# Performance work log

Measured on AMD Instinct MI355X. Metric: run time of the kernel, lower is better.

## Reference

```python
import jax, jax.numpy as jnp
import numpy as np
import math

NUM_BUCKETS = 32
MAX_DISTANCE = 128
N_HEADS = 16
D_KV = 64


def _relative_position_bucket(relative_position, num_buckets=NUM_BUCKETS, max_distance=MAX_DISTANCE):
    # bidirectional (encoder) variant
    num_buckets //= 2
    relative_buckets = (relative_position > 0).astype(jnp.int32) * num_buckets
    rp = jnp.abs(relative_position)
    max_exact = num_buckets // 2
    is_small = rp < max_exact
    rp_large = max_exact + (
        jnp.log(jnp.maximum(rp, 1).astype(jnp.float32) / max_exact)
        / math.log(max_distance / max_exact)
        * (num_buckets - max_exact)
    ).astype(jnp.int32)
    rp_large = jnp.minimum(rp_large, num_buckets - 1)
    return relative_buckets + jnp.where(is_small, rp, rp_large)


def compute_bias(rel_bias, q_len, k_len):
    ctx = jnp.arange(q_len)[:, None]
    mem = jnp.arange(k_len)[None, :]
    buckets = _relative_position_bucket(mem - ctx)          # [q, k]
    values = rel_bias[buckets]                               # [q, k, h]
    return jnp.transpose(values, (2, 0, 1))[None]            # [1, h, q, k]


def setup_inputs() -> dict:
    key = jax.random.key(0)
    ks = jax.random.split(key, 6)
    d_model, inner = 1024, N_HEADS * D_KV
    s = 0.02
    return {
        "hidden_states": jax.random.normal(ks[0], (2, 2048, d_model), jnp.float32),
        "Wq": jax.random.normal(ks[1], (d_model, inner), jnp.float32) * s,
        "Wk": jax.random.normal(ks[2], (d_model, inner), jnp.float32) * s,
        "Wv": jax.random.normal(ks[3], (d_model, inner), jnp.float32) * s,
        "Wo": jax.random.normal(ks[4], (inner, d_model), jnp.float32) * s,
        "rel_bias": jax.random.normal(ks[5], (NUM_BUCKETS, N_HEADS), jnp.float32) * s,
    }


def reference(hidden_states, Wq, Wk, Wv, Wo, rel_bias):
    B, S, D = hidden_states.shape

    def split_heads(x):  # [B,S,inner] -> [B,H,S,dk]
        return x.reshape(B, S, N_HEADS, D_KV).transpose(0, 2, 1, 3)

    q = split_heads(hidden_states @ Wq)
    k = split_heads(hidden_states @ Wk)
    v = split_heads(hidden_states @ Wv)

    # T5 does NOT scale by 1/sqrt(d_kv)
    scores = jnp.einsum("bhqd,bhkd->bhqk", q, k)
    scores = scores + compute_bias(rel_bias, S, S)
    attn = jax.nn.softmax(scores, axis=-1)
    ctx = jnp.einsum("bhqk,bhkd->bhqd", attn, v)
    ctx = ctx.transpose(0, 2, 1, 3).reshape(B, S, N_HEADS * D_KV)
    return ctx @ Wo
```

## Files before the change

### kernel.cpp

```cpp
#include <hip/hip_runtime.h>
#include <hip/hip_bf16.h>

typedef __bf16 bf16x8 __attribute__((ext_vector_type(8)));
typedef __bf16 bf16x4 __attribute__((ext_vector_type(4)));
typedef float floatx4 __attribute__((ext_vector_type(4)));
using bf16 = __hip_bfloat16;

#define S_    2048
#define NHEAD 16
#define LOG2E 1.4426950408889634f

__device__ __forceinline__ void load_lds16(const bf16* g, void* lds) {
  __builtin_amdgcn_global_load_lds((const __attribute__((address_space(1))) void*)g,
                                   (__attribute__((address_space(3))) void*)lds, 16, 0, 0);
}

__global__ void prep_kernel(const float* __restrict__ hidden,
                            const float* __restrict__ wq, const float* __restrict__ wk,
                            const float* __restrict__ wv, const float* __restrict__ wo,
                            const float* __restrict__ rel_bias,
                            bf16* __restrict__ hbf, bf16* __restrict__ wt_qkv,
                            bf16* __restrict__ wt_o, float* __restrict__ tab) {
  __shared__ bf16 tile[32][33];
  int bid = blockIdx.x;
  if (bid < 4096) {
    int i = (bid * 256 + threadIdx.x) * 4;
    float4 v = *(const float4*)(hidden + i);
    bf16 o[4] = {__float2bfloat16(v.x), __float2bfloat16(v.y),
                 __float2bfloat16(v.z), __float2bfloat16(v.w)};
    *(uint2*)(hbf + i) = *(const uint2*)o;
  } else if (bid < 8192) {
    int r = bid - 4096;
    int mat = r >> 10;
    int rem = r & 1023;
    int n0 = (rem & 31) * 32, k0 = (rem >> 5) * 32;
    int tx = threadIdx.x & 31, ty = threadIdx.x >> 5;
    const float* src = (mat == 0) ? wq : (mat == 1) ? wk : (mat == 2) ? wv : wo;
    bf16* dst = (mat == 3) ? wt_o : wt_qkv + mat * 1024 * 1024;
#pragma unroll
    for (int j = 0; j < 32; j += 8)
      tile[ty + j][tx] = __float2bfloat16(src[(k0 + ty + j) * 1024 + n0 + tx]);
    __syncthreads();
#pragma unroll
    for (int j = 0; j < 32; j += 8)
      dst[(n0 + ty + j) * 1024 + k0 + tx] = tile[tx][ty + j];
  } else {
    int idx = (bid - 8192) * 256 + threadIdx.x;
    int h = idx >> 12, j = idx & 4095;
    int delta = j - 2048;
    int rb = (delta > 0) ? 16 : 0;
    int rpa = delta < 0 ? -delta : delta;
    int bsmall;
    if (rpa < 8) {
      bsmall = rpa;
    } else {
      int lg = 25 - __clz(rpa * rpa);
      bsmall = 8 + lg;
      if (bsmall > 15) bsmall = 15;
    }
    tab[idx] = rel_bias[(rb + bsmall) * 16 + h] * LOG2E;
  }
}

__global__ __launch_bounds__(256) void gemm_qkv_kernel(const bf16* __restrict__ A,
                                                       const bf16* __restrict__ Bt,
                                                       bf16* __restrict__ qh,
                                                       bf16* __restrict__ kf,
                                                       bf16* __restrict__ vf) {
  const int K = 1024;
  __shared__ bf16 As[128 * 32];
  __shared__ bf16 Bs[128 * 32];
  int t = threadIdx.x;
  int m0 = blockIdx.y * 128, n0 = blockIdx.x * 128;
  int w = t >> 6, lane = t & 63, ln = lane & 15, quad = lane >> 4;
  int wr = w >> 1, wc = w & 1;
  floatx4 acc[4][4];
  floatx4 zero = {0.f, 0.f, 0.f, 0.f};
#pragma unroll
  for (int i = 0; i < 4; i++)
#pragma unroll
    for (int j = 0; j < 4; j++) acc[i][j] = zero;

  int r = t >> 2, c = (t & 3) * 8;
  const bf16* Ag = A + (long)(m0 + r) * K + c;
  const bf16* Bg = Bt + (long)(n0 + r) * K + c;
  char* ldsA0 = (char*)As + w * 1024;
  char* ldsA1 = ldsA0 + 4096;
  char* ldsB0 = (char*)Bs + w * 1024;
  char* ldsB1 = ldsB0 + 4096;

  for (int k0 = 0; k0 < K; k0 += 32) {
    load_lds16(Ag + k0, ldsA0);
    load_lds16(Ag + (long)64 * K + k0, ldsA1);
    load_lds16(Bg + k0, ldsB0);
    load_lds16(Bg + (long)64 * K + k0, ldsB1);
    __syncthreads();
    bf16x8 af[4], bfv[4];
#pragma unroll
    for (int i = 0; i < 4; i++)
      af[i] = *(const bf16x8*)&As[(wr * 64 + i * 16 + ln) * 32 + quad * 8];
#pragma unroll
    for (int j = 0; j < 4; j++)
      bfv[j] = *(const bf16x8*)&Bs[(wc * 64 + j * 16 + ln) * 32 + quad * 8];
#pragma unroll
    for (int i = 0; i < 4; i++)
#pragma unroll
      for (int j = 0; j < 4; j++)
        acc[i][j] = __builtin_amdgcn_mfma_f32_16x16x32_bf16(af[i], bfv[j], acc[i][j], 0, 0, 0);
    __syncthreads();
  }

  int nb = n0 + wc * 64;
  int type = nb >> 10, h = (nb >> 6) & 15;
  int b = (m0 >> 11);
  int sl0 = (m0 & 2047) + wr * 64;
  long bhbase = (long)((b * 16 + h)) * 131072;

  if (type == 0) {
#pragma unroll
    for (int i = 0; i < 4; i++)
#pragma unroll
      for (int j = 0; j < 4; j++) {
        int d = j * 16 + ln;
#pragma unroll
        for (int rr = 0; rr < 4; rr++) {
          int s = sl0 + i * 16 + quad * 4 + rr;
          qh[bhbase + (long)s * 64 + d] = __float2bfloat16(acc[i][j][rr]);
        }
      }
  } else if (type == 1) {
#pragma unroll
    for (int i = 0; i < 4; i++)
#pragma unroll
      for (int j = 0; j < 4; j++) {
        int d = j * 16 + ln;
        int dpart = (d >> 5) * 512 + ((d >> 3) & 3) * 128 + (d & 7);
        int kb = (sl0 + i * 16) * 64;
#pragma unroll
        for (int rr = 0; rr < 4; rr++)
          kf[bhbase + kb + dpart + (quad * 4 + rr) * 8] = __float2bfloat16(acc[i][j][rr]);
      }
  } else {
#pragma unroll
    for (int i = 0; i < 4; i++)
#pragma unroll
      for (int j = 0; j < 4; j++) {
        int off = (sl0 + (i >> 1) * 32) * 64 + j * 512 +
                  ((quad >> 1) + ((i & 1) << 1)) * 128 + ln * 8 + (quad & 1) * 4;
        bf16x4 pk = {(__bf16)acc[i][j][0], (__bf16)acc[i][j][1],
                     (__bf16)acc[i][j][2], (__bf16)acc[i][j][3]};
        *(bf16x4*)(vf + bhbase + off) = pk;
      }
  }
}

__global__ __launch_bounds__(128, 2) void attn_kernel(const bf16* __restrict__ qh,
                                                      const bf16* __restrict__ kf,
                                                      const bf16* __restrict__ vf,
                                                      const float* __restrict__ btab,
                                                      bf16* __restrict__ ctx) {
  __shared__ char PsRaw[2 * 4096];
  __shared__ char KV[2][16384];
  int t = threadIdx.x, w = t >> 6, lane = t & 63, ln = lane & 15, quad = lane >> 4;
  int bh = blockIdx.x, b = bh >> 4, h = bh & 15;
  int qw = blockIdx.y * 64 + w * 32;

  const bf16* qbase = qh + (long)bh * S_ * 64;
  const bf16* kfb = kf + (long)bh * S_ * 64;
  const bf16* vfb = vf + (long)bh * S_ * 64;
  const float* bt = btab + h * 4096;
  char* myPs = PsRaw + w * 4096;
  int lbo = quad * 256 + ln * 16;

  bf16x8 Qf[2][2];
#pragma unroll
  for (int qt = 0; qt < 2; qt++) {
    const bf16* qr = qbase + (long)(qw + qt * 16 + ln) * 64;
    Qf[qt][0] = *(const bf16x8*)(qr + quad * 8);
    Qf[qt][1] = *(const bf16x8*)(qr + 32 + quad * 8);
  }

  float cneg = bt[0], cpos = bt[4095];
  float l_acc[2] = {0.f, 0.f};
  floatx4 o[2][4];
  floatx4 zero = {0.f, 0.f, 0.f, 0.f};
#pragma unroll
  for (int qt = 0; qt < 2; qt++)
#pragma unroll
    for (int dt = 0; dt < 4; dt++) o[qt][dt] = zero;

  {
    const bf16* kg = kfb + t * 8;
    const bf16* vg = vfb + t * 8;
#pragma unroll
    for (int c = 0; c < 4; c++) {
      load_lds16(kg + c * 1024, KV[0] + c * 2048 + w * 1024);
      load_lds16(vg + c * 1024, KV[0] + 8192 + c * 2048 + w * 1024);
    }
  }

  int pb = 0;
  for (int k0 = 0; k0 < S_; k0 += 64) {
    __syncthreads();
    int kn = k0 + 64;
    if (kn < S_) {
      const bf16* kg = kfb + (long)kn * 64 + t * 8;
      const bf16* vg = vfb + (long)kn * 64 + t * 8;
      char* nb_ = KV[pb ^ 1];
#pragma unroll
      for (int c = 0; c < 4; c++) {
        load_lds16(kg + c * 1024, nb_ + c * 2048 + w * 1024);
        load_lds16(vg + c * 1024, nb_ + 8192 + c * 2048 + w * 1024);
      }
    }

    const char* bK = KV[pb];
    const char* bV = KV[pb] + 8192;
    bf16x8 Kr[4][2], Vr[4][2];
#pragma unroll
    for (int tile = 0; tile < 4; tile++) {
      Kr[tile][0] = *(const bf16x8*)(bK + tile * 2048 + lbo);
      Kr[tile][1] = *(const bf16x8*)(bK + tile * 2048 + 1024 + lbo);
    }
#pragma unroll
    for (int f = 0; f < 2; f++)
#pragma unroll
      for (int dt = 0; dt < 4; dt++)
        Vr[dt][f] = *(const bf16x8*)(bV + f * 4096 + dt * 1024 + lbo);

    floatx4 st[2][4];
#pragma unroll
    for (int qt = 0; qt < 2; qt++)
#pragma unroll
      for (int tile = 0; tile < 4; tile++) {
        st[qt][tile] = __builtin_amdgcn_mfma_f32_16x16x32_bf16(Kr[tile][0], Qf[qt][0], zero, 0, 0, 0);
        st[qt][tile] = __builtin_amdgcn_mfma_f32_16x16x32_bf16(Kr[tile][1], Qf[qt][1], st[qt][tile], 0, 0, 0);
      }

#pragma unroll
    for (int qt = 0; qt < 2; qt++) {
      int qwt = qw + qt * 16;
      char* Ps = myPs + qt * 2048;
      bool near = (k0 > qwt - 192) && (k0 < qwt + 144);
      if (near) {
#pragma unroll
        for (int tile = 0; tile < 4; tile++) {
          int bidx = k0 + tile * 16 + quad * 4 - (qwt + ln) + 2048;
          float p0 = __builtin_amdgcn_exp2f(fmaf(st[qt][tile][0], LOG2E, bt[bidx + 0]));
          float p1 = __builtin_amdgcn_exp2f(fmaf(st[qt][tile][1], LOG2E, bt[bidx + 1]));
          float p2 = __builtin_amdgcn_exp2f(fmaf(st[qt][tile][2], LOG2E, bt[bidx + 2]));
          float p3 = __builtin_amdgcn_exp2f(fmaf(st[qt][tile][3], LOG2E, bt[bidx + 3]));
          l_acc[qt] += (p0 + p1) + (p2 + p3);
          bf16x4 pk = {(__bf16)p0, (__bf16)p1, (__bf16)p2, (__bf16)p3};
          int chunk = tile * 2 + (quad >> 1);
          *(bf16x4*)(Ps + (ln * 8 + (chunk ^ (ln & 7))) * 16 + (quad & 1) * 8) = pk;
        }
      } else {
        float cb = (k0 > qwt) ? cpos : cneg;
#pragma unroll
        for (int tile = 0; tile < 4; tile++) {
          float p0 = __builtin_amdgcn_exp2f(fmaf(st[qt][tile][0], LOG2E, cb));
          float p1 = __builtin_amdgcn_exp2f(fmaf(st[qt][tile][1], LOG2E, cb));
          float p2 = __builtin_amdgcn_exp2f(fmaf(st[qt][tile][2], LOG2E, cb));
          float p3 = __builtin_amdgcn_exp2f(fmaf(st[qt][tile][3], LOG2E, cb));
          l_acc[qt] += (p0 + p1) + (p2 + p3);
          bf16x4 pk = {(__bf16)p0, (__bf16)p1, (__bf16)p2, (__bf16)p3};
          int chunk = tile * 2 + (quad >> 1);
          *(bf16x4*)(Ps + (ln * 8 + (chunk ^ (ln & 7))) * 16 + (quad & 1) * 8) = pk;
        }
      }
    }

#pragma unroll
    for (int qt = 0; qt < 2; qt++) {
      char* Ps = myPs + qt * 2048;
      bf16x8 Pf0 = *(const bf16x8*)(Ps + (ln * 8 + (quad ^ (ln & 7))) * 16);
      bf16x8 Pf1 = *(const bf16x8*)(Ps + (ln * 8 + ((4 + quad) ^ (ln & 7))) * 16);
#pragma unroll
      for (int dt = 0; dt < 4; dt++) {
        o[qt][dt] = __builtin_amdgcn_mfma_f32_16x16x32_bf16(Pf0, Vr[dt][0], o[qt][dt], 0, 0, 0);
        o[qt][dt] = __builtin_amdgcn_mfma_f32_16x16x32_bf16(Pf1, Vr[dt][1], o[qt][dt], 0, 0, 0);
      }
    }

    pb ^= 1;
  }

#pragma unroll
  for (int qt = 0; qt < 2; qt++) {
    float la = l_acc[qt];
    la += __shfl_xor(la, 16);
    la += __shfl_xor(la, 32);
#pragma unroll
    for (int rr = 0; rr < 4; rr++) {
      float linv = 1.0f / __shfl(la, quad * 4 + rr);
      int q = qw + qt * 16 + quad * 4 + rr;
#pragma unroll
      for (int dt = 0; dt < 4; dt++)
        ctx[(long)(b * S_ + q) * 1024 + h * 64 + dt * 16 + ln] =
            __float2bfloat16(o[qt][dt][rr] * linv);
    }
  }
}

__global__ __launch_bounds__(256) void gemm_bt_kernel(const bf16* __restrict__ A,
                                                      const bf16* __restrict__ Bt,
                                                      float* __restrict__ C,
                                                      int M, int N, int K) {
  __shared__ bf16 As[128 * 32];
  __shared__ bf16 Bs[128 * 32];
  int t = threadIdx.x;
  int m0 = blockIdx.y * 128, n0 = blockIdx.x * 128;
  int w = t >> 6, lane = t & 63, ln = lane & 15, quad = lane >> 4;
  int wr = w >> 1, wc = w & 1;
  floatx4 acc[4][4];
  floatx4 zero = {0.f, 0.f, 0.f, 0.f};
#pragma unroll
  for (int i = 0; i < 4; i++)
#pragma unroll
    for (int j = 0; j < 4; j++) acc[i][j] = zero;

  int r = t >> 2, c = (t & 3) * 8;
  const bf16* Ag = A + (long)(m0 + r) * K + c;
  const bf16* Bg = Bt + (long)(n0 + r) * K + c;
  char* ldsA0 = (char*)As + w * 1024;
  char* ldsA1 = ldsA0 + 4096;
  char* ldsB0 = (char*)Bs + w * 1024;
  char* ldsB1 = ldsB0 + 4096;

  for (int k0 = 0; k0 < K; k0 += 32) {
    load_lds16(Ag + k0, ldsA0);
    load_lds16(Ag + (long)64 * K + k0, ldsA1);
    load_lds16(Bg + k0, ldsB0);
    load_lds16(Bg + (long)64 * K + k0, ldsB1);
    __syncthreads();
    bf16x8 af[4], bfv[4];
#pragma unroll
    for (int i = 0; i < 4; i++)
      af[i] = *(const bf16x8*)&As[(wr * 64 + i * 16 + ln) * 32 + quad * 8];
#pragma unroll
    for (int j = 0; j < 4; j++)
      bfv[j] = *(const bf16x8*)&Bs[(wc * 64 + j * 16 + ln) * 32 + quad * 8];
#pragma unroll
    for (int i = 0; i < 4; i++)
#pragma unroll
      for (int j = 0; j < 4; j++)
        acc[i][j] = __builtin_amdgcn_mfma_f32_16x16x32_bf16(af[i], bfv[j], acc[i][j], 0, 0, 0);
    __syncthreads();
  }

#pragma unroll
  for (int i = 0; i < 4; i++)
#pragma unroll
    for (int j = 0; j < 4; j++)
#pragma unroll
      for (int rr = 0; rr < 4; rr++)
        C[(long)(m0 + wr * 64 + i * 16 + quad * 4 + rr) * N + n0 + wc * 64 + j * 16 + ln] =
            acc[i][j][rr];
}

extern "C" void kernel_launch(void* const* d_in, const int* in_sizes, int n_in,
                              void* d_out, int out_size, void* d_ws, size_t ws_size,
                              hipStream_t stream) {
  (void)in_sizes; (void)n_in; (void)out_size; (void)ws_size;
  const float* hidden   = (const float*)d_in[0];
  const float* Wq       = (const float*)d_in[1];
  const float* Wk       = (const float*)d_in[2];
  const float* Wv       = (const float*)d_in[3];
  const float* Wo       = (const float*)d_in[4];
  const float* rel_bias = (const float*)d_in[5];

  char* ws = (char*)d_ws;
  bf16*  hbf    = (bf16*)(ws + 0);
  bf16*  wt_qkv = (bf16*)(ws + 8388608);
  bf16*  wt_o   = (bf16*)(ws + 14680064);
  float* btab   = (float*)(ws + 16777216);
  bf16*  qh     = (bf16*)(ws + 17039360);
  bf16*  kf     = (bf16*)(ws + 25427968);
  bf16*  vf     = (bf16*)(ws + 33816576);
  bf16*  ctx    = (bf16*)(ws + 42205184);

  prep_kernel<<<dim3(8448), dim3(256), 0, stream>>>(hidden, Wq, Wk, Wv, Wo, rel_bias,
                                                    hbf, wt_qkv, wt_o, btab);
  gemm_qkv_kernel<<<dim3(24, 32), dim3(256), 0, stream>>>(hbf, wt_qkv, qh, kf, vf);
  attn_kernel<<<dim3(32, 32), dim3(128), 0, stream>>>(qh, kf, vf, btab, ctx);
  gemm_bt_kernel<<<dim3(8, 32), dim3(256), 0, stream>>>(ctx, wt_o, (float*)d_out, 4096, 1024, 1024);
}
```

Baseline: 200.7 us.

## Switch attention to 32x32x16 MFMA with register-resident P via permlane swap

Rewrites the attention inner loop to use 32x32x16 bf16 MFMA tiles instead of 16x16x32. The probabilities stay in registers, converted with v_cvt_pk_bf16_f32 and rearranged with v_permlane32_swap into the A-operand layout, so the LDS round trip for P goes away. The K/V pre-layouts written by the projection kernel change to match the new operand fragment order. The trade-offs are larger accumulators (two floatx16 per wave) and a coarser near-diagonal test, which may raise register pressure.

```diff
diff --git a/kernel.cpp b/kernel.cpp
--- a/kernel.cpp
+++ b/kernel.cpp
@@ -4,6 +4,7 @@
 typedef __bf16 bf16x8 __attribute__((ext_vector_type(8)));
 typedef __bf16 bf16x4 __attribute__((ext_vector_type(4)));
 typedef float floatx4 __attribute__((ext_vector_type(4)));
+typedef float floatx16 __attribute__((ext_vector_type(16)));
 using bf16 = __hip_bfloat16;
 
 #define S_    2048
@@ -133,20 +134,19 @@
     for (int i = 0; i < 4; i++)
 #pragma unroll
       for (int j = 0; j < 4; j++) {
-        int d = j * 16 + ln;
-        int dpart = (d >> 5) * 512 + ((d >> 3) & 3) * 128 + (d & 7);
-        int kb = (sl0 + i * 16) * 64;
+        long base = bhbase + sl0 * 64 + (i >> 1) * 2048 + j * 512 + (ln >> 3) * 256 +
+                    (i & 1) * 128 + quad * 32 + (ln & 7);
 #pragma unroll
         for (int rr = 0; rr < 4; rr++)
-          kf[bhbase + kb + dpart + (quad * 4 + rr) * 8] = __float2bfloat16(acc[i][j][rr]);
+          kf[base + rr * 8] = __float2bfloat16(acc[i][j][rr]);
       }
   } else {
 #pragma unroll
     for (int i = 0; i < 4; i++)
 #pragma unroll
       for (int j = 0; j < 4; j++) {
-        int off = (sl0 + (i >> 1) * 32) * 64 + j * 512 +
-                  ((quad >> 1) + ((i & 1) << 1)) * 128 + ln * 8 + (quad & 1) * 4;
+        long off = sl0 * 64 + i * 1024 + (j >> 1) * 512 + (quad >> 1) * 256 +
+                   ((j & 1) * 16 + ln) * 8 + (quad & 1) * 4;
         bf16x4 pk = {(__bf16)acc[i][j][0], (__bf16)acc[i][j][1],
                      (__bf16)acc[i][j][2], (__bf16)acc[i][j][3]};
         *(bf16x4*)(vf + bhbase + off) = pk;
@@ -159,9 +159,9 @@
                                                       const bf16* __restrict__ vf,
                                                       const float* __restrict__ btab,
                                                       bf16* __restrict__ ctx) {
-  __shared__ char PsRaw[2 * 4096];
   __shared__ char KV[2][16384];
-  int t = threadIdx.x, w = t >> 6, lane = t & 63, ln = lane & 15, quad = lane >> 4;
+  int t = threadIdx.x, w = t >> 6, lane = t & 63;
+  int l31 = lane & 31, h5 = lane >> 5;
   int bh = blockIdx.x, b = bh >> 4, h = bh & 15;
   int qw = blockIdx.y * 64 + w * 32;
 
@@ -169,25 +169,17 @@
   const bf16* kfb = kf + (long)bh * S_ * 64;
   const bf16* vfb = vf + (long)bh * S_ * 64;
   const float* bt = btab + h * 4096;
-  char* myPs = PsRaw + w * 4096;
-  int lbo = quad * 256 + ln * 16;
-
-  bf16x8 Qf[2][2];
-#pragma unroll
-  for (int qt = 0; qt < 2; qt++) {
-    const bf16* qr = qbase + (long)(qw + qt * 16 + ln) * 64;
-    Qf[qt][0] = *(const bf16x8*)(qr + quad * 8);
-    Qf[qt][1] = *(const bf16x8*)(qr + 32 + quad * 8);
-  }
+
+  bf16x8 Qf[4];
+#pragma unroll
+  for (int ds = 0; ds < 4; ds++)
+    Qf[ds] = *(const bf16x8*)(qbase + (long)(qw + l31) * 64 + ds * 16 + h5 * 8);
 
   float cneg = bt[0], cpos = bt[4095];
-  float l_acc[2] = {0.f, 0.f};
-  floatx4 o[2][4];
-  floatx4 zero = {0.f, 0.f, 0.f, 0.f};
-#pragma unroll
-  for (int qt = 0; qt < 2; qt++)
-#pragma unroll
-    for (int dt = 0; dt < 4; dt++) o[qt][dt] = zero;
+  float l_acc = 0.f;
+  floatx16 zf = {0.f, 0.f, 0.f, 0.f, 0.f, 0.f, 0.f, 0.f,
+                 0.f, 0.f, 0.f, 0.f, 0.f, 0.f, 0.f, 0.f};
+  floatx16 o0 = zf, o1 = zf;
 
   {
     const bf16* kg = kfb + t * 8;
@@ -204,8 +196,8 @@
     __syncthreads();
     int kn = k0 + 64;
     if (kn < S_) {
-      const bf16* kg = kfb + (long)kn * 64 + t * 8;
-      const bf16* vg = vfb + (long)kn * 64 + t * 8;
+      const bf16* kg = kfb + kn * 64 + t * 8;
+      const bf16* vg = vfb + kn * 64 + t * 8;
       char* nb_ = KV[pb ^ 1];
 #pragma unroll
       for (int c = 0; c < 4; c++) {
@@ -216,90 +208,83 @@
 
     const char* bK = KV[pb];
     const char* bV = KV[pb] + 8192;
-    bf16x8 Kr[4][2], Vr[4][2];
-#pragma unroll
-    for (int tile = 0; tile < 4; tile++) {
-      Kr[tile][0] = *(const bf16x8*)(bK + tile * 2048 + lbo);
-      Kr[tile][1] = *(const bf16x8*)(bK + tile * 2048 + 1024 + lbo);
-    }
-#pragma unroll
-    for (int f = 0; f < 2; f++)
-#pragma unroll
-      for (int dt = 0; dt < 4; dt++)
-        Vr[dt][f] = *(const bf16x8*)(bV + f * 4096 + dt * 1024 + lbo);
-
-    floatx4 st[2][4];
-#pragma unroll
-    for (int qt = 0; qt < 2; qt++)
-#pragma unroll
-      for (int tile = 0; tile < 4; tile++) {
-        st[qt][tile] = __builtin_amdgcn_mfma_f32_16x16x32_bf16(Kr[tile][0], Qf[qt][0], zero, 0, 0, 0);
-        st[qt][tile] = __builtin_amdgcn_mfma_f32_16x16x32_bf16(Kr[tile][1], Qf[qt][1], st[qt][tile], 0, 0, 0);
-      }
-
-#pragma unroll
-    for (int qt = 0; qt < 2; qt++) {
-      int qwt = qw + qt * 16;
-      char* Ps = myPs + qt * 2048;
-      bool near = (k0 > qwt - 192) && (k0 < qwt + 144);
+
+    floatx16 st0 = zf, st1 = zf;
+#pragma unroll
+    for (int ds = 0; ds < 4; ds++) {
+      bf16x8 Kf0 = *(const bf16x8*)(bK + ds * 1024 + lane * 16);
+      st0 = __builtin_amdgcn_mfma_f32_32x32x16_bf16(Kf0, Qf[ds], st0, 0, 0, 0);
+    }
+#pragma unroll
+    for (int ds = 0; ds < 4; ds++) {
+      bf16x8 Kf1 = *(const bf16x8*)(bK + 4096 + ds * 1024 + lane * 16);
+      st1 = __builtin_amdgcn_mfma_f32_32x32x16_bf16(Kf1, Qf[ds], st1, 0, 0, 0);
+    }
+
+    bf16x8 Af[4];
+    bool near = (k0 > qw - 192) && (k0 < qw + 160);
+#pragma unroll
+    for (int s = 0; s < 2; s++) {
+      const floatx16 stv = s ? st1 : st0;
+      float p[16];
       if (near) {
-#pragma unroll
-        for (int tile = 0; tile < 4; tile++) {
-          int bidx = k0 + tile * 16 + quad * 4 - (qwt + ln) + 2048;
-          float p0 = __builtin_amdgcn_exp2f(fmaf(st[qt][tile][0], LOG2E, bt[bidx + 0]));
-          float p1 = __builtin_amdgcn_exp2f(fmaf(st[qt][tile][1], LOG2E, bt[bidx + 1]));
-          float p2 = __builtin_amdgcn_exp2f(fmaf(st[qt][tile][2], LOG2E, bt[bidx + 2]));
-          float p3 = __builtin_amdgcn_exp2f(fmaf(st[qt][tile][3], LOG2E, bt[bidx + 3]));
-          l_acc[qt] += (p0 + p1) + (p2 + p3);
-          bf16x4 pk = {(__bf16)p0, (__bf16)p1, (__bf16)p2, (__bf16)p3};
-          int chunk = tile * 2 + (quad >> 1);
-          *(bf16x4*)(Ps + (ln * 8 + (chunk ^ (ln & 7))) * 16 + (quad & 1) * 8) = pk;
-        }
+        int kb = k0 + s * 32 + 4 * h5 - (qw + l31) + 2048;
+#pragma unroll
+        for (int r = 0; r < 16; r++)
+          p[r] = __builtin_amdgcn_exp2f(
+              fmaf(stv[r], LOG2E, bt[kb + (r & 3) + 8 * (r >> 2)]));
       } else {
-        float cb = (k0 > qwt) ? cpos : cneg;
-#pragma unroll
-        for (int tile = 0; tile < 4; tile++) {
-          float p0 = __builtin_amdgcn_exp2f(fmaf(st[qt][tile][0], LOG2E, cb));
-          float p1 = __builtin_amdgcn_exp2f(fmaf(st[qt][tile][1], LOG2E, cb));
-          float p2 = __builtin_amdgcn_exp2f(fmaf(st[qt][tile][2], LOG2E, cb));
-          float p3 = __builtin_amdgcn_exp2f(fmaf(st[qt][tile][3], LOG2E, cb));
-          l_acc[qt] += (p0 + p1) + (p2 + p3);
-          bf16x4 pk = {(__bf16)p0, (__bf16)p1, (__bf16)p2, (__bf16)p3};
-          int chunk = tile * 2 + (quad >> 1);
-          *(bf16x4*)(Ps + (ln * 8 + (chunk ^ (ln & 7))) * 16 + (quad & 1) * 8) = pk;
-        }
-      }
-    }
-
-#pragma unroll
-    for (int qt = 0; qt < 2; qt++) {
-      char* Ps = myPs + qt * 2048;
-      bf16x8 Pf0 = *(const bf16x8*)(Ps + (ln * 8 + (quad ^ (ln & 7))) * 16);
-      bf16x8 Pf1 = *(const bf16x8*)(Ps + (ln * 8 + ((4 + quad) ^ (ln & 7))) * 16);
-#pragma unroll
-      for (int dt = 0; dt < 4; dt++) {
-        o[qt][dt] = __builtin_amdgcn_mfma_f32_16x16x32_bf16(Pf0, Vr[dt][0], o[qt][dt], 0, 0, 0);
-        o[qt][dt] = __builtin_amdgcn_mfma_f32_16x16x32_bf16(Pf1, Vr[dt][1], o[qt][dt], 0, 0, 0);
-      }
+        float cb = (k0 > qw) ? cpos : cneg;
+#pragma unroll
+        for (int r = 0; r < 16; r++)
+          p[r] = __builtin_amdgcn_exp2f(fmaf(stv[r], LOG2E, cb));
+      }
+      float a0 = (p[0] + p[1]) + (p[2] + p[3]);
+      float a1 = (p[4] + p[5]) + (p[6] + p[7]);
+      float a2 = (p[8] + p[9]) + (p[10] + p[11]);
+      float a3 = (p[12] + p[13]) + (p[14] + p[15]);
+      l_acc += (a0 + a1) + (a2 + a3);
+
+      unsigned d[8];
+#pragma unroll
+      for (int i = 0; i < 8; i++)
+        asm("v_cvt_pk_bf16_f32 %0, %1, %2" : "=v"(d[i]) : "v"(p[2 * i]), "v"(p[2 * i + 1]));
+      unsigned w0 = d[0], w2 = d[2];
+      asm("v_permlane32_swap_b32 %0, %1" : "+v"(w0), "+v"(w2));
+      unsigned w1 = d[1], w3 = d[3];
+      asm("v_permlane32_swap_b32 %0, %1" : "+v"(w1), "+v"(w3));
+      unsigned w4 = d[4], w6 = d[6];
+      asm("v_permlane32_swap_b32 %0, %1" : "+v"(w4), "+v"(w6));
+      unsigned w5 = d[5], w7 = d[7];
+      asm("v_permlane32_swap_b32 %0, %1" : "+v"(w5), "+v"(w7));
+      union { unsigned u[4]; bf16x8 v; } a0u, a1u;
+      a0u.u[0] = w0; a0u.u[1] = w1; a0u.u[2] = w2; a0u.u[3] = w3;
+      a1u.u[0] = w4; a1u.u[1] = w5; a1u.u[2] = w6; a1u.u[3] = w7;
+      Af[s * 2 + 0] = a0u.v;
+      Af[s * 2 + 1] = a1u.v;
+    }
+
+#pragma unroll
+    for (int tt = 0; tt < 4; tt++) {
+      bf16x8 Vf0 = *(const bf16x8*)(bV + tt * 2048 + lane * 16);
+      bf16x8 Vf1 = *(const bf16x8*)(bV + tt * 2048 + 1024 + lane * 16);
+      o0 = __builtin_amdgcn_mfma_f32_32x32x16_bf16(Af[tt], Vf0, o0, 0, 0, 0);
+      o1 = __builtin_amdgcn_mfma_f32_32x32x16_bf16(Af[tt], Vf1, o1, 0, 0, 0);
     }
 
     pb ^= 1;
   }
 
-#pragma unroll
-  for (int qt = 0; qt < 2; qt++) {
-    float la = l_acc[qt];
-    la += __shfl_xor(la, 16);
-    la += __shfl_xor(la, 32);
-#pragma unroll
-    for (int rr = 0; rr < 4; rr++) {
-      float linv = 1.0f / __shfl(la, quad * 4 + rr);
-      int q = qw + qt * 16 + quad * 4 + rr;
-#pragma unroll
-      for (int dt = 0; dt < 4; dt++)
-        ctx[(long)(b * S_ + q) * 1024 + h * 64 + dt * 16 + ln] =
-            __float2bfloat16(o[qt][dt][rr] * linv);
-    }
+  l_acc += __shfl_xor(l_acc, 32);
+  float linv = 1.0f / l_acc;
+#pragma unroll
+  for (int r = 0; r < 16; r++) {
+    int qrow = (r & 3) + 8 * (r >> 2) + 4 * h5;
+    float lv = __shfl(linv, qrow);
+    int q = qw + qrow;
+    long base = (long)(b * S_ + q) * 1024 + h * 64 + l31;
+    ctx[base] = __float2bfloat16(o0[r] * lv);
+    ctx[base + 32] = __float2bfloat16(o1[r] * lv);
   }
 }
 
```

Result: no change. 201.8 us (+0.6%).
